# Kernel tuning notes

Measured on AMD Instinct MI355X. Metric: run time of the kernel, lower is better.

## Reference

```python
import jax, jax.numpy as jnp
import numpy as np
from jax import lax

B, S, E, CC, H, NH, K = 8, 2048, 128, 256, 256, 8, 7
HD = H // NH  # head dim = 32


def setup_inputs() -> dict:
    key = jax.random.key(0)
    ks = jax.random.split(key, 16)
    x = jax.random.normal(ks[0], (B, S, E), dtype=jnp.float32)
    lengths = jax.random.randint(ks[1], (B,), S // 2, S + 1)
    mask = (jnp.arange(S)[None, :] < lengths[:, None])  # contiguous prefix padding mask
    sc = 0.02
    return {
        "x": x,
        "mask": mask,
        "conv_w": jax.random.normal(ks[2], (CC, E, K), dtype=jnp.float32) * sc,
        "conv_b": jnp.zeros((CC,), jnp.float32),
        "wq": jax.random.normal(ks[3], (CC, H), dtype=jnp.float32) * sc,
        "bq": jnp.zeros((H,), jnp.float32),
        "wk": jax.random.normal(ks[4], (CC, H), dtype=jnp.float32) * sc,
        "bk": jnp.zeros((H,), jnp.float32),
        "wv": jax.random.normal(ks[5], (CC, H), dtype=jnp.float32) * sc,
        "bv": jnp.zeros((H,), jnp.float32),
        "fc_w": jax.random.normal(ks[6], (H, CC), dtype=jnp.float32) * sc,
        "fc_b": jnp.zeros((CC,), jnp.float32),
        "ln_g": jnp.ones((CC,), jnp.float32),
        "ln_b": jnp.zeros((CC,), jnp.float32),
        "gamma": jnp.float32(0.5),
        "std_param": jnp.float32(0.2),
    }


def _penalty(mask, gamma, std_param):
    # (B, S, S) Gaussian penalty, nonzero only in the valid_len x valid_len block
    valid_len = mask.sum(axis=-1).astype(jnp.float32)  # (B,)
    idx = jnp.arange(S, dtype=jnp.float32)
    valid = (jnp.arange(S)[None, :] < mask.sum(axis=-1)[:, None]).astype(jnp.float32)  # (B,S)
    norm_pos = (idx[None, :] + 1.0) / (valid_len[:, None] + 1.0)  # (B,S)
    std = jnp.clip(std_param, 0.01, 0.5)
    base = jnp.exp(-((norm_pos - 0.5) ** 2) / (2.0 * std * std))
    pvec = base * (jnp.exp(gamma) - 1.0) * valid  # (B,S)
    pen = 0.5 * (pvec[:, :, None] + pvec[:, None, :])
    return pen * valid[:, :, None] * valid[:, None, :]


def reference(x, mask, conv_w, conv_b, wq, bq, wk, bk, wv, bv, fc_w, fc_b, ln_g, ln_b, gamma, std_param):
    # Conv1d frontend: (B,S,E) -> (B,E,S) -> conv -> relu -> (B,S,CC)
    xt = jnp.transpose(x, (0, 2, 1))
    y = lax.conv_general_dilated(xt, conv_w, window_strides=(1,), padding=[(K // 2, K // 2)])
    y = jax.nn.relu(y + conv_b[None, :, None])
    h = jnp.transpose(y, (0, 2, 1))  # (B,S,CC)

    q = (h @ wq + bq).reshape(B, S, NH, HD).transpose(0, 2, 1, 3)
    k = (h @ wk + bk).reshape(B, S, NH, HD).transpose(0, 2, 1, 3)
    v = (h @ wv + bv).reshape(B, S, NH, HD).transpose(0, 2, 1, 3)

    scores = jnp.einsum('bnqd,bnkd->bnqk', q, k) / np.sqrt(HD).astype(np.float32)
    scores = scores - _penalty(mask, gamma, std_param)[:, None, :, :]
    scores = jnp.where(mask[:, None, None, :], scores, jnp.float32(-1e10))
    probs = jax.nn.softmax(scores, axis=-1)
    ctx = jnp.einsum('bnqk,bnkd->bnqd', probs, v)
    ctx = ctx.transpose(0, 2, 1, 3).reshape(B, S, H)
    out = ctx @ fc_w + fc_b

    z = h + out
    mu = z.mean(-1, keepdims=True)
    var = ((z - mu) ** 2).mean(-1, keepdims=True)
    return (z - mu) / jnp.sqrt(var + 1e-5) * ln_g + ln_b
```

## Files before the change

### kernel.cpp

```cpp
#include <hip/hip_runtime.h>
#include <hip/hip_bf16.h>

#define B_ 8
#define S_ 2048
#define E_ 128
#define CC_ 256
#define H_ 256
#define NH_ 8
#define HD_ 32
#define KW_ 7

typedef __attribute__((ext_vector_type(8))) short bf16x8;
typedef __attribute__((ext_vector_type(2))) float f32x2;
typedef __attribute__((ext_vector_type(4))) float f32x4;
typedef __attribute__((ext_vector_type(16))) float f32x16;

#define QSCALE_ (0.17677669529663687f * 1.4426950408889634f)
#define CPEN_   0.7213475204444817f

static __device__ __forceinline__ unsigned short f2bf(float f) {
    __hip_bfloat16 h = __float2bfloat16(f);
    return *(unsigned short*)&h;
}
static __device__ __forceinline__ float bf2f(unsigned short u) {
    __hip_bfloat16 h = *(__hip_bfloat16*)&u;
    return __bfloat162float(h);
}
static __device__ __forceinline__ void perm32swap(unsigned& a, unsigned& b) {
    asm volatile("s_nop 1\n\tv_permlane32_swap_b32 %0, %1" : "+v"(a), "+v"(b));
}

__global__ __launch_bounds__(256) void prep_kernel(
    const float* __restrict__ cw, const float* __restrict__ wq,
    const float* __restrict__ wk, const float* __restrict__ wv,
    const float* __restrict__ fw, const void* __restrict__ mask,
    const float* __restrict__ gamma_p, const float* __restrict__ std_p,
    unsigned short* __restrict__ wre2, unsigned short* __restrict__ wqkv2,
    unsigned short* __restrict__ wf2, float* __restrict__ ctab,
    int* __restrict__ lenv)
{
    __shared__ int cnt[256];
    const int blk = blockIdx.x, tid = threadIdx.x;

    if (blk < 896) {
        int i = blk * 256 + tid;
        int kl = i & 31, cc = (i >> 5) & 255, eb = (i >> 13) & 3, kk = i >> 15;
        wre2[i] = f2bf(cw[cc * (E_ * KW_) + (eb * 32 + kl) * KW_ + kk]);
    } else if (blk < 1664) {
        int i = (blk - 896) * 256 + tid;
        int kl = i & 31, col = (i >> 5) & 255, kb = (i >> 13) & 7, m = i >> 16;
        const float* W = (m == 0) ? wq : (m == 1) ? wk : wv;
        wqkv2[i] = f2bf(W[(kb * 32 + kl) * H_ + col]);
    } else if (blk < 1920) {
        int i = (blk - 1664) * 256 + tid;
        int kl = i & 31, col = (i >> 5) & 255, kb = i >> 13;
        wf2[i] = f2bf(fw[(kb * 32 + kl) * CC_ + col]);
    } else {
        int b = blk - 1920;

        uint32_t w0 = ((const uint32_t*)mask)[0];
        int mode = 0;
        if (w0 == 0x01010101u) mode = 1;
        else if (w0 == 0x3F803F80u) mode = 2;
        else if (w0 == 0x3F800000u) mode = 3;

        int c = 0;
        for (int s = tid; s < S_; s += 256) {
            bool vv;
            size_t i = (size_t)b * S_ + s;
            if (mode == 0)      vv = ((const int*)mask)[i] != 0;
            else if (mode == 1) vv = ((const unsigned char*)mask)[i] != 0;
            else if (mode == 2) vv = (((const unsigned short*)mask)[i] & 0x7FFFu) != 0;
            else                vv = ((const float*)mask)[i] != 0.f;
            c += vv ? 1 : 0;
        }
        cnt[tid] = c;
        __syncthreads();
        for (int off = 128; off > 0; off >>= 1) {
            if (tid < off) cnt[tid] += cnt[tid + off];
            __syncthreads();
        }
        int L = cnt[0];
        if (tid == 0) lenv[b] = L;

        float Lf = (float)L;
        float gamma = gamma_p[0];
        float sd = std_p[0];
        sd = fminf(fmaxf(sd, 0.01f), 0.5f);
        float scale = expf(gamma) - 1.f;
        float inv2s2 = 1.f / (2.f * sd * sd);
        float* row0 = ctab + (size_t)b * 2 * S_;
        float* row1 = row0 + S_;
        for (int s = tid; s < S_; s += 256) {
            float np = (s + 1.f) / (Lf + 1.f);
            float e = np - 0.5f;
            float base = expf(-(e * e) * inv2s2);
            bool vkk = s < L;
            row0[s] = vkk ? 0.f : -1e10f;
            row1[s] = vkk ? (-CPEN_ * base * scale) : -1e10f;
        }
    }
}

__global__ __launch_bounds__(256) void front_kernel(
    const float* __restrict__ x, const unsigned short* __restrict__ wre2,
    const float* __restrict__ cb, const unsigned short* __restrict__ wqkv2,
    const float* __restrict__ bq, const float* __restrict__ bk,
    const float* __restrict__ bv, unsigned short* __restrict__ hb,
    unsigned short* __restrict__ qo, unsigned short* __restrict__ ko,
    unsigned short* __restrict__ vo)
{
    __shared__ __align__(16) char smem[64 * 264 * 2];
    short (*xl)[136] = (short(*)[136])smem;
    short (*Al)[264] = (short(*)[264])smem;

    const int tid = threadIdx.x, wave = tid >> 6, lane = tid & 63;
    const int l15 = lane & 15, l4 = lane >> 4;
    const int s0 = blockIdx.x * 64, b = blockIdx.y;

    for (int idx = tid; idx < 70 * 32; idx += 256) {
        int row = idx >> 5, c4 = idx & 31;
        int pos = s0 - 3 + row;
        float4 v = {0.f, 0.f, 0.f, 0.f};
        if (pos >= 0 && pos < S_)
            v = *(const float4*)(x + ((size_t)b * S_ + pos) * E_ + c4 * 4);
        short* p = &xl[row][c4 * 4];
        p[0] = (short)f2bf(v.x); p[1] = (short)f2bf(v.y);
        p[2] = (short)f2bf(v.z); p[3] = (short)f2bf(v.w);
    }
    __syncthreads();

    f32x4 acc[4][4];
#pragma unroll
    for (int i = 0; i < 4; i++)
#pragma unroll
        for (int j = 0; j < 4; j++) acc[i][j] = (f32x4){0.f, 0.f, 0.f, 0.f};

#pragma unroll 1
    for (int kk = 0; kk < KW_; kk++) {
#pragma unroll
        for (int eb = 0; eb < 4; eb++) {
            const unsigned short* wp =
                wre2 + (((size_t)(kk * 4 + eb) * 256 + wave * 64 + l15) * 32) + l4 * 8;
            bf16x8 af[4], bfr[4];
#pragma unroll
            for (int ct = 0; ct < 4; ct++)
                bfr[ct] = *(const bf16x8*)(wp + ct * 512);
#pragma unroll
            for (int rt = 0; rt < 4; rt++)
                af[rt] = *(const bf16x8*)(&xl[rt * 16 + l15 + kk][eb * 32 + l4 * 8]);
#pragma unroll
            for (int rt = 0; rt < 4; rt++)
#pragma unroll
                for (int ct = 0; ct < 4; ct++)
                    acc[rt][ct] = __builtin_amdgcn_mfma_f32_16x16x32_bf16(
                        af[rt], bfr[ct], acc[rt][ct], 0, 0, 0);
        }
    }
    __syncthreads();

#pragma unroll
    for (int ct = 0; ct < 4; ct++) {
        int col = wave * 64 + ct * 16 + l15;
        float bias = cb[col];
#pragma unroll
        for (int rt = 0; rt < 4; rt++)
#pragma unroll
            for (int r = 0; r < 4; r++) {
                float v0 = acc[rt][ct][r] + bias;
                v0 = v0 > 0.f ? v0 : 0.f;
                Al[rt * 16 + l4 * 4 + r][col] = (short)f2bf(v0);
            }
    }
    __syncthreads();

    for (int idx = tid; idx < 64 * 32; idx += 256) {
        int row = idx >> 5, c8 = idx & 31;
        *(bf16x8*)(hb + ((size_t)b * S_ + s0 + row) * CC_ + c8 * 8) =
            *(const bf16x8*)(&Al[row][c8 * 8]);
    }

#pragma unroll 1
    for (int m = 0; m < 3; m++) {
        f32x4 qacc[4][4];
#pragma unroll
        for (int i = 0; i < 4; i++)
#pragma unroll
            for (int j = 0; j < 4; j++) qacc[i][j] = (f32x4){0.f, 0.f, 0.f, 0.f};

#pragma unroll 1
        for (int kb8 = 0; kb8 < 8; kb8++) {
            const unsigned short* wp =
                wqkv2 + (((size_t)(m * 8 + kb8) * 256 + wave * 64 + l15) * 32) + l4 * 8;
            bf16x8 af[4], bfr[4];
#pragma unroll
            for (int ct = 0; ct < 4; ct++)
                bfr[ct] = *(const bf16x8*)(wp + ct * 512);
#pragma unroll
            for (int rt = 0; rt < 4; rt++)
                af[rt] = *(const bf16x8*)(&Al[rt * 16 + l15][kb8 * 32 + l4 * 8]);
#pragma unroll
            for (int rt = 0; rt < 4; rt++)
#pragma unroll
                for (int ct = 0; ct < 4; ct++)
                    qacc[rt][ct] = __builtin_amdgcn_mfma_f32_16x16x32_bf16(
                        af[rt], bfr[ct], qacc[rt][ct], 0, 0, 0);
        }

        const float* bias_p = (m == 0) ? bq : (m == 1) ? bk : bv;
        unsigned short* O = (m == 0) ? qo : (m == 1) ? ko : vo;
        const float oscale = (m == 0) ? QSCALE_ : 1.f;
#pragma unroll
        for (int ct = 0; ct < 4; ct++) {
            int col = wave * 64 + ct * 16 + l15;
            float bias = bias_p[col];
            int n = col >> 5, d = col & 31;
#pragma unroll
            for (int rt = 0; rt < 4; rt++)
#pragma unroll
                for (int r = 0; r < 4; r++) {
                    int row = s0 + rt * 16 + l4 * 4 + r;
                    O[(((size_t)b * NH_ + n) * S_ + row) * HD_ + d] =
                        f2bf((qacc[rt][ct][r] + bias) * oscale);
                }
        }
    }
}

__global__ __launch_bounds__(256) void attn_mfma_kernel(
    const unsigned short* __restrict__ q, const unsigned short* __restrict__ k,
    const unsigned short* __restrict__ v, const float* __restrict__ ctab,
    const int* __restrict__ lenv, unsigned short* __restrict__ ctxb)
{
    __shared__ short Kt[2][128][40];
    __shared__ short Vt[2][32][136];
    __shared__ __align__(16) float ctC[2][2][128];

    const int tid = threadIdx.x;
    const int wave = tid >> 6, lane = tid & 63;
    const int r31 = lane & 31, hi = lane >> 5;
    const int hi8 = hi * 8, hi4 = hi * 4;

    const int idx = blockIdx.x;
    const int b = (idx >> 3) & 7, n = idx & 7, qt = idx >> 6;
    const int qrow = qt * 128 + wave * 32 + r31;
    const int L = lenv[b];
    const int nt = (L + 127) >> 7;

    const size_t head = ((size_t)b * NH_ + n) * S_;
    const unsigned short* qbase = q + head * HD_;
    const unsigned short* kbase = k + head * HD_;
    const unsigned short* vbase = v + head * HD_;
    const float* ct0 = ctab + (size_t)b * 2 * S_;
    const float* ct1 = ct0 + S_;

    bf16x8 qf0 = *(const bf16x8*)(qbase + (size_t)qrow * HD_ + hi8);
    bf16x8 qf1 = *(const bf16x8*)(qbase + (size_t)qrow * HD_ + 16 + hi8);
    const int crow = (qrow < L) ? 1 : 0;

    f32x16 acc;
#pragma unroll
    for (int r = 0; r < 16; r++) acc[r] = 0.f;
    float m_r = -1e30f, l_r = 0.f;

    const int krow = tid >> 1, kch = (tid & 1) * 16;
    const int d7x2 = 2 * (r31 & 7);
    const int vc = krow >> 3, vk7 = krow & 7;

    bf16x8 kreg0, kreg1, va, vb;
    float c0r = 0.f, c1r = 0.f;

    kreg0 = *(const bf16x8*)(kbase + (size_t)krow * HD_ + kch);
    kreg1 = *(const bf16x8*)(kbase + (size_t)krow * HD_ + kch + 8);
    va    = *(const bf16x8*)(vbase + (size_t)krow * HD_ + kch);
    vb    = *(const bf16x8*)(vbase + (size_t)krow * HD_ + kch + 8);
    if (tid < 128) { c0r = ct0[tid]; c1r = ct1[tid]; }
    {
        *(bf16x8*)(&Kt[0][krow][kch])     = kreg0;
        *(bf16x8*)(&Kt[0][krow][kch + 8]) = kreg1;
#pragma unroll
        for (int i = 0; i < 8; i++) {
            int d0 = kch + i, d1 = kch + 8 + i;
            Vt[0][d0][((((vc - 2 * (d0 & 7)) & 7) | (vc & 8)) << 3) + vk7] = va[i];
            Vt[0][d1][((((vc - 2 * (d1 & 7)) & 7) | (vc & 8)) << 3) + vk7] = vb[i];
        }
        if (tid < 128) { ctC[0][0][tid] = c0r; ctC[0][1][tid] = c1r; }
    }
    __syncthreads();

#pragma unroll 1
    for (int t = 0; t < nt; t++) {
        const int cur = t & 1;
        const int knext = (t + 1) << 7;
        const bool more = (t + 1 < nt);

        if (more) {
            kreg0 = *(const bf16x8*)(kbase + (size_t)(knext + krow) * HD_ + kch);
            kreg1 = *(const bf16x8*)(kbase + (size_t)(knext + krow) * HD_ + kch + 8);
            va    = *(const bf16x8*)(vbase + (size_t)(knext + krow) * HD_ + kch);
            vb    = *(const bf16x8*)(vbase + (size_t)(knext + krow) * HD_ + kch + 8);
            if (tid < 128) { c0r = ct0[knext + tid]; c1r = ct1[knext + tid]; }
        }

        __builtin_amdgcn_s_setprio(1);
        f32x16 sc[4];
#pragma unroll
        for (int t4 = 0; t4 < 4; t4++) {
            bf16x8 kf0 = *(const bf16x8*)(&Kt[cur][t4 * 32 + r31][hi8]);
            bf16x8 kf1 = *(const bf16x8*)(&Kt[cur][t4 * 32 + r31][16 + hi8]);
            f32x16 c0;
#pragma unroll
            for (int g = 0; g < 4; g++) {
                f32x4 cp = *(const f32x4*)(&ctC[cur][crow][t4 * 32 + g * 8 + hi4]);
#pragma unroll
                for (int j = 0; j < 4; j++) c0[g * 4 + j] = cp[j];
            }
            f32x16 s1 = __builtin_amdgcn_mfma_f32_32x32x16_bf16(kf0, qf0, c0, 0, 0, 0);
            sc[t4] = __builtin_amdgcn_mfma_f32_32x32x16_bf16(kf1, qf1, s1, 0, 0, 0);
        }
        __builtin_amdgcn_s_setprio(0);

        float pmx = -1e30f;
#pragma unroll
        for (int t4 = 0; t4 < 4; t4++)
#pragma unroll
            for (int r = 0; r < 16; r += 2)
                pmx = fmaxf(pmx, fmaxf(sc[t4][r], sc[t4][r + 1]));
        pmx = fmaxf(pmx, __shfl_xor(pmx, 32, 64));

        float alpha = 1.f;
        if (!__all(pmx <= m_r + 8.f)) {
            float mn = fmaxf(m_r, pmx);
            alpha = exp2f(m_r - mn);
            m_r = mn;
#pragma unroll
            for (int r = 0; r < 16; r++) acc[r] *= alpha;
        }

        f32x2 rs2 = {0.f, 0.f};
        const f32x2 m2 = {m_r, m_r};
        unsigned pk[4][8];
#pragma unroll
        for (int t4 = 0; t4 < 4; t4++) {
            unsigned U[8];
#pragma unroll
            for (int j = 0; j < 8; j++) {
                f32x2 s2 = { sc[t4][2 * j], sc[t4][2 * j + 1] };
                s2 = s2 - m2;
                f32x2 p2 = { exp2f(s2.x), exp2f(s2.y) };
                rs2 += p2;
                U[j] = (unsigned)f2bf(p2.x) | ((unsigned)f2bf(p2.y) << 16);
            }
            perm32swap(U[0], U[2]);
            perm32swap(U[1], U[3]);
            perm32swap(U[4], U[6]);
            perm32swap(U[5], U[7]);
            pk[t4][0] = U[0]; pk[t4][1] = U[1]; pk[t4][2] = U[2]; pk[t4][3] = U[3];
            pk[t4][4] = U[4]; pk[t4][5] = U[5]; pk[t4][6] = U[6]; pk[t4][7] = U[7];
        }
        float rs = rs2.x + rs2.y;
        rs += __shfl_xor(rs, 32, 64);
        l_r = l_r * alpha + rs;

        __builtin_amdgcn_s_setprio(1);
#pragma unroll
        for (int t4 = 0; t4 < 4; t4++) {
            union { unsigned u[4]; bf16x8 v8; } pb0, pb1;
            pb0.u[0] = pk[t4][0]; pb0.u[1] = pk[t4][1];
            pb0.u[2] = pk[t4][2]; pb0.u[3] = pk[t4][3];
            pb1.u[0] = pk[t4][4]; pb1.u[1] = pk[t4][5];
            pb1.u[2] = pk[t4][6]; pb1.u[3] = pk[t4][7];
            int c0i = t4 * 4 + hi, c1i = t4 * 4 + 2 + hi;
            bf16x8 vf0 = *(const bf16x8*)(&Vt[cur][r31][(((c0i - d7x2) & 7) | (c0i & 8)) << 3]);
            bf16x8 vf1 = *(const bf16x8*)(&Vt[cur][r31][(((c1i - d7x2) & 7) | (c1i & 8)) << 3]);
            acc = __builtin_amdgcn_mfma_f32_32x32x16_bf16(vf0, pb0.v8, acc, 0, 0, 0);
            acc = __builtin_amdgcn_mfma_f32_32x32x16_bf16(vf1, pb1.v8, acc, 0, 0, 0);
        }
        __builtin_amdgcn_s_setprio(0);

        if (more) {
            const int nxt = cur ^ 1;
            *(bf16x8*)(&Kt[nxt][krow][kch])     = kreg0;
            *(bf16x8*)(&Kt[nxt][krow][kch + 8]) = kreg1;
#pragma unroll
            for (int i = 0; i < 8; i++) {
                int d0 = kch + i, d1 = kch + 8 + i;
                Vt[nxt][d0][((((vc - 2 * (d0 & 7)) & 7) | (vc & 8)) << 3) + vk7] = va[i];
                Vt[nxt][d1][((((vc - 2 * (d1 & 7)) & 7) | (vc & 8)) << 3) + vk7] = vb[i];
            }
            if (tid < 128) { ctC[nxt][0][tid] = c0r; ctC[nxt][1][tid] = c1r; }
            __syncthreads();
        }
    }

    float inv = 1.f / l_r;
    size_t obase = ((size_t)b * S_ + qrow) * H_ + n * HD_;
#pragma unroll
    for (int g = 0; g < 4; g++)
#pragma unroll
        for (int w = 0; w < 2; w++) {
            unsigned uo = (unsigned)f2bf(acc[g * 4 + w * 2] * inv) |
                          ((unsigned)f2bf(acc[g * 4 + w * 2 + 1] * inv) << 16);
            int d = 8 * g + hi4 + 2 * w;
            *(unsigned*)(ctxb + obase + d) = uo;
        }
}

__global__ __launch_bounds__(256) void fc_ln_mfma_kernel(
    const unsigned short* __restrict__ ctxb, const unsigned short* __restrict__ hb,
    const unsigned short* __restrict__ wf2, const float* __restrict__ fb,
    const float* __restrict__ g, const float* __restrict__ bbias,
    float* __restrict__ out)
{
    const int tid = threadIdx.x, wave = tid >> 6, lane = tid & 63;
    const int l15 = lane & 15, l4 = lane >> 4;
    const int s0 = blockIdx.x * 64, b = blockIdx.y;
    const int arow = s0 + wave * 16 + l15;

    bf16x8 af[8];
#pragma unroll
    for (int kb = 0; kb < 8; kb++)
        af[kb] = *(const bf16x8*)(ctxb + (size_t)((size_t)b * S_ + arow) * H_ + kb * 32 + l4 * 8);

    f32x4 acc[16];
#pragma unroll
    for (int ct = 0; ct < 16; ct++) acc[ct] = (f32x4){0.f, 0.f, 0.f, 0.f};

#pragma unroll 1
    for (int kb = 0; kb < 8; kb++) {
        const unsigned short* wp = wf2 + ((size_t)kb * 256 + l15) * 32 + l4 * 8;
#pragma unroll
        for (int ct = 0; ct < 16; ct++) {
            bf16x8 bfr = *(const bf16x8*)(wp + ct * 512);
            acc[ct] = __builtin_amdgcn_mfma_f32_16x16x32_bf16(af[kb], bfr, acc[ct], 0, 0, 0);
        }
    }

    float fbias[16];
#pragma unroll
    for (int ct = 0; ct < 16; ct++) fbias[ct] = fb[ct * 16 + l15];

#pragma unroll
    for (int r = 0; r < 4; r++) {
        int row = s0 + wave * 16 + l4 * 4 + r;
        size_t ro = ((size_t)b * S_ + row) * CC_;
        float z[16];
        float sum = 0.f;
#pragma unroll
        for (int ct = 0; ct < 16; ct++) {
            float zz = acc[ct][r] + fbias[ct] + bf2f(hb[ro + ct * 16 + l15]);
            z[ct] = zz;
            sum += zz;
        }
#pragma unroll
        for (int off = 1; off < 16; off <<= 1) sum += __shfl_xor(sum, off, 64);
        float mu = sum * (1.f / 256.f);
        float vs = 0.f;
#pragma unroll
        for (int ct = 0; ct < 16; ct++) {
            float d = z[ct] - mu;
            z[ct] = d;
            vs += d * d;
        }
#pragma unroll
        for (int off = 1; off < 16; off <<= 1) vs += __shfl_xor(vs, off, 64);
        float inv = rsqrtf(vs * (1.f / 256.f) + 1e-5f);
#pragma unroll
        for (int ct = 0; ct < 16; ct++) {
            int col = ct * 16 + l15;
            out[ro + col] = z[ct] * inv * g[col] + bbias[col];
        }
    }
}

extern "C" void kernel_launch(void* const* d_in, const int* in_sizes, int n_in,
                              void* d_out, int out_size, void* d_ws, size_t ws_size,
                              hipStream_t stream)
{
    const float* x      = (const float*)d_in[0];
    const void*  mask   = d_in[1];
    const float* conv_w = (const float*)d_in[2];
    const float* conv_b = (const float*)d_in[3];
    const float* wq     = (const float*)d_in[4];
    const float* bq     = (const float*)d_in[5];
    const float* wk     = (const float*)d_in[6];
    const float* bk     = (const float*)d_in[7];
    const float* wv     = (const float*)d_in[8];
    const float* bv     = (const float*)d_in[9];
    const float* fc_w   = (const float*)d_in[10];
    const float* fc_b   = (const float*)d_in[11];
    const float* ln_g   = (const float*)d_in[12];
    const float* ln_b   = (const float*)d_in[13];
    const float* gamma  = (const float*)d_in[14];
    const float* stdp   = (const float*)d_in[15];

    char* ws = (char*)d_ws;
    const size_t MB = 1024 * 1024;
    unsigned short* hb    = (unsigned short*)(ws);
    unsigned short* qb    = (unsigned short*)(ws + 8 * MB);
    unsigned short* kb    = (unsigned short*)(ws + 16 * MB);
    unsigned short* vb    = (unsigned short*)(ws + 24 * MB);
    unsigned short* ctxb  = (unsigned short*)(ws + 32 * MB);
    float*          ctab  = (float*)(ws + 40 * MB);
    int*            lenv  = (int*)(ws + 40 * MB + 256 * 1024);
    unsigned short* wre2  = (unsigned short*)(ws + 41 * MB);
    unsigned short* wqkv2 = (unsigned short*)(ws + 42 * MB);
    unsigned short* wf2   = (unsigned short*)(ws + 43 * MB);

    prep_kernel<<<1928, 256, 0, stream>>>(conv_w, wq, wk, wv, fc_w, mask,
                                          gamma, stdp, wre2, wqkv2, wf2,
                                          ctab, lenv);
    dim3 g2(S_ / 64, B_);
    front_kernel<<<g2, 256, 0, stream>>>(x, wre2, conv_b, wqkv2, bq, bk, bv,
                                         hb, qb, kb, vb);
    attn_mfma_kernel<<<1024, 256, 0, stream>>>(qb, kb, vb, ctab, lenv, ctxb);
    fc_ln_mfma_kernel<<<g2, 256, 0, stream>>>(ctxb, hb, wf2, fc_b, ln_g, ln_b,
                                              (float*)d_out);
}
```

Measured before the change: 218.1 us.

## Use 512-thread attention blocks covering 256 query rows per K/V tile

The attention kernel now launches 8-wave blocks that each handle 256 query rows, so every K/V tile staged in shared memory is reused by twice as many query rows. With twice the threads, each one loads a single 8-element chunk of K and V. The grid becomes a 3D (query-tile, head, batch) launch, which also changes the block scheduling order. The softmax packing is rewritten with scalar exp2 instead of paired float2 math. Larger blocks halve the number of blocks and may lower occupancy or increase barrier stalls.

```diff
diff --git a/kernel.cpp b/kernel.cpp
--- a/kernel.cpp
+++ b/kernel.cpp
@@ -11,7 +11,6 @@
 #define KW_ 7
 
 typedef __attribute__((ext_vector_type(8))) short bf16x8;
-typedef __attribute__((ext_vector_type(2))) float f32x2;
 typedef __attribute__((ext_vector_type(4))) float f32x4;
 typedef __attribute__((ext_vector_type(16))) float f32x16;
 
@@ -227,7 +226,7 @@
     }
 }
 
-__global__ __launch_bounds__(256) void attn_mfma_kernel(
+__global__ __launch_bounds__(512) void attn_mfma_kernel(
     const unsigned short* __restrict__ q, const unsigned short* __restrict__ k,
     const unsigned short* __restrict__ v, const float* __restrict__ ctab,
     const int* __restrict__ lenv, unsigned short* __restrict__ ctxb)
@@ -241,9 +240,8 @@
     const int r31 = lane & 31, hi = lane >> 5;
     const int hi8 = hi * 8, hi4 = hi * 4;
 
-    const int idx = blockIdx.x;
-    const int b = (idx >> 3) & 7, n = idx & 7, qt = idx >> 6;
-    const int qrow = qt * 128 + wave * 32 + r31;
+    const int qt = blockIdx.x, n = blockIdx.y, b = blockIdx.z;
+    const int qrow = qt * 256 + wave * 32 + r31;
     const int L = lenv[b];
     const int nt = (L + 127) >> 7;
 
@@ -263,26 +261,22 @@
     for (int r = 0; r < 16; r++) acc[r] = 0.f;
     float m_r = -1e30f, l_r = 0.f;
 
-    const int krow = tid >> 1, kch = (tid & 1) * 16;
+    const int krow = tid >> 2, kch = (tid & 3) * 8;
     const int d7x2 = 2 * (r31 & 7);
     const int vc = krow >> 3, vk7 = krow & 7;
 
-    bf16x8 kreg0, kreg1, va, vb;
+    bf16x8 kreg, va;
     float c0r = 0.f, c1r = 0.f;
 
-    kreg0 = *(const bf16x8*)(kbase + (size_t)krow * HD_ + kch);
-    kreg1 = *(const bf16x8*)(kbase + (size_t)krow * HD_ + kch + 8);
-    va    = *(const bf16x8*)(vbase + (size_t)krow * HD_ + kch);
-    vb    = *(const bf16x8*)(vbase + (size_t)krow * HD_ + kch + 8);
+    kreg = *(const bf16x8*)(kbase + (size_t)krow * HD_ + kch);
+    va   = *(const bf16x8*)(vbase + (size_t)krow * HD_ + kch);
     if (tid < 128) { c0r = ct0[tid]; c1r = ct1[tid]; }
     {
-        *(bf16x8*)(&Kt[0][krow][kch])     = kreg0;
-        *(bf16x8*)(&Kt[0][krow][kch + 8]) = kreg1;
+        *(bf16x8*)(&Kt[0][krow][kch]) = kreg;
 #pragma unroll
         for (int i = 0; i < 8; i++) {
-            int d0 = kch + i, d1 = kch + 8 + i;
+            int d0 = kch + i;
             Vt[0][d0][((((vc - 2 * (d0 & 7)) & 7) | (vc & 8)) << 3) + vk7] = va[i];
-            Vt[0][d1][((((vc - 2 * (d1 & 7)) & 7) | (vc & 8)) << 3) + vk7] = vb[i];
         }
         if (tid < 128) { ctC[0][0][tid] = c0r; ctC[0][1][tid] = c1r; }
     }
@@ -295,10 +289,8 @@
         const bool more = (t + 1 < nt);
 
         if (more) {
-            kreg0 = *(const bf16x8*)(kbase + (size_t)(knext + krow) * HD_ + kch);
-            kreg1 = *(const bf16x8*)(kbase + (size_t)(knext + krow) * HD_ + kch + 8);
-            va    = *(const bf16x8*)(vbase + (size_t)(knext + krow) * HD_ + kch);
-            vb    = *(const bf16x8*)(vbase + (size_t)(knext + krow) * HD_ + kch + 8);
+            kreg = *(const bf16x8*)(kbase + (size_t)(knext + krow) * HD_ + kch);
+            va   = *(const bf16x8*)(vbase + (size_t)(knext + krow) * HD_ + kch);
             if (tid < 128) { c0r = ct0[knext + tid]; c1r = ct1[knext + tid]; }
         }
 
@@ -337,28 +329,31 @@
             for (int r = 0; r < 16; r++) acc[r] *= alpha;
         }
 
-        f32x2 rs2 = {0.f, 0.f};
-        const f32x2 m2 = {m_r, m_r};
+        float rs = 0.f;
         unsigned pk[4][8];
 #pragma unroll
         for (int t4 = 0; t4 < 4; t4++) {
-            unsigned U[8];
-#pragma unroll
-            for (int j = 0; j < 8; j++) {
-                f32x2 s2 = { sc[t4][2 * j], sc[t4][2 * j + 1] };
-                s2 = s2 - m2;
-                f32x2 p2 = { exp2f(s2.x), exp2f(s2.y) };
-                rs2 += p2;
-                U[j] = (unsigned)f2bf(p2.x) | ((unsigned)f2bf(p2.y) << 16);
+            float p[16];
+#pragma unroll
+            for (int r = 0; r < 16; r++) {
+                p[r] = exp2f(sc[t4][r] - m_r);
+                rs += p[r];
             }
-            perm32swap(U[0], U[2]);
-            perm32swap(U[1], U[3]);
-            perm32swap(U[4], U[6]);
-            perm32swap(U[5], U[7]);
-            pk[t4][0] = U[0]; pk[t4][1] = U[1]; pk[t4][2] = U[2]; pk[t4][3] = U[3];
-            pk[t4][4] = U[4]; pk[t4][5] = U[5]; pk[t4][6] = U[6]; pk[t4][7] = U[7];
-        }
-        float rs = rs2.x + rs2.y;
+            unsigned U00 = (unsigned)f2bf(p[0])  | ((unsigned)f2bf(p[1])  << 16);
+            unsigned U01 = (unsigned)f2bf(p[2])  | ((unsigned)f2bf(p[3])  << 16);
+            unsigned U10 = (unsigned)f2bf(p[4])  | ((unsigned)f2bf(p[5])  << 16);
+            unsigned U11 = (unsigned)f2bf(p[6])  | ((unsigned)f2bf(p[7])  << 16);
+            unsigned U20 = (unsigned)f2bf(p[8])  | ((unsigned)f2bf(p[9])  << 16);
+            unsigned U21 = (unsigned)f2bf(p[10]) | ((unsigned)f2bf(p[11]) << 16);
+            unsigned U30 = (unsigned)f2bf(p[12]) | ((unsigned)f2bf(p[13]) << 16);
+            unsigned U31 = (unsigned)f2bf(p[14]) | ((unsigned)f2bf(p[15]) << 16);
+            perm32swap(U00, U10);
+            perm32swap(U01, U11);
+            perm32swap(U20, U30);
+            perm32swap(U21, U31);
+            pk[t4][0] = U00; pk[t4][1] = U01; pk[t4][2] = U10; pk[t4][3] = U11;
+            pk[t4][4] = U20; pk[t4][5] = U21; pk[t4][6] = U30; pk[t4][7] = U31;
+        }
         rs += __shfl_xor(rs, 32, 64);
         l_r = l_r * alpha + rs;
 
@@ -380,13 +375,11 @@
 
         if (more) {
             const int nxt = cur ^ 1;
-            *(bf16x8*)(&Kt[nxt][krow][kch])     = kreg0;
-            *(bf16x8*)(&Kt[nxt][krow][kch + 8]) = kreg1;
+            *(bf16x8*)(&Kt[nxt][krow][kch]) = kreg;
 #pragma unroll
             for (int i = 0; i < 8; i++) {
-                int d0 = kch + i, d1 = kch + 8 + i;
+                int d0 = kch + i;
                 Vt[nxt][d0][((((vc - 2 * (d0 & 7)) & 7) | (vc & 8)) << 3) + vk7] = va[i];
-                Vt[nxt][d1][((((vc - 2 * (d1 & 7)) & 7) | (vc & 8)) << 3) + vk7] = vb[i];
             }
             if (tid < 128) { ctC[nxt][0][tid] = c0r; ctC[nxt][1][tid] = c1r; }
             __syncthreads();
@@ -513,7 +506,8 @@
     dim3 g2(S_ / 64, B_);
     front_kernel<<<g2, 256, 0, stream>>>(x, wre2, conv_b, wqkv2, bq, bk, bv,
                                          hb, qb, kb, vb);
-    attn_mfma_kernel<<<1024, 256, 0, stream>>>(qb, kb, vb, ctab, lenv, ctxb);
+    dim3 ag(S_ / 256, NH_, B_);
+    attn_mfma_kernel<<<ag, 512, 0, stream>>>(qb, kb, vb, ctab, lenv, ctxb);
     fc_ln_mfma_kernel<<<g2, 256, 0, stream>>>(ctxb, hb, wf2, fc_b, ln_g, ln_b,
                                               (float*)d_out);
 }
```

Result: faster. 197.9 us (-9.2%).
